# Kernel optimization log

Hardware: AMD Instinct MI355X
Metric: run time of the kernel (lower is better)

Reference implementation:

```python
import jax, jax.numpy as jnp
import numpy as np

T, H = 2048, 1024          # tokens, hidden_size
NH, NKV, D = 16, 4, 64     # heads, kv heads, head_dim
E, F = 8, 1024             # experts, intermediate_size
TOPK = 1
EPS = 1e-5
THETA = 500000.0
SCALE = D ** -0.5


def rmsnorm(x, w=None, eps=EPS):
    # fp32 accumulation like vLLM RMSNorm
    v = jnp.mean(x.astype(jnp.float32) ** 2, axis=-1, keepdims=True)
    y = x.astype(jnp.float32) * jax.lax.rsqrt(v + eps)
    y = y.astype(x.dtype)
    return y * w if w is not None else y


def setup_inputs() -> dict:
    key = jax.random.key(0)
    ks = jax.random.split(key, 12)
    s = 1.0 / np.sqrt(H)
    sf = 1.0 / np.sqrt(F)
    return {
        "positions": jnp.arange(T, dtype=jnp.int32),
        "hidden_states": jax.random.normal(ks[0], (T, H), jnp.float32),
        "ln1_w": jnp.ones((H,), jnp.float32),
        "ln2_w": jnp.ones((H,), jnp.float32),
        "wqkv": jax.random.normal(ks[1], (H, (NH + 2 * NKV) * D), jnp.float32) * s,
        "wo": jax.random.normal(ks[2], (NH * D, H), jnp.float32) * s,
        "router_w": jax.random.normal(ks[3], (H, E), jnp.float32) * s,
        "w_gate": jax.random.normal(ks[4], (E, H, F), jnp.float32) * s,
        "w_up": jax.random.normal(ks[5], (E, H, F), jnp.float32) * s,
        "w_down": jax.random.normal(ks[6], (E, F, H), jnp.float32) * sf,
        "sh_gate": jax.random.normal(ks[7], (H, F), jnp.float32) * s,
        "sh_up": jax.random.normal(ks[8], (H, F), jnp.float32) * s,
        "sh_down": jax.random.normal(ks[9], (F, H), jnp.float32) * sf,
    }


def reference(positions, hidden_states, ln1_w, ln2_w, wqkv, wo, router_w,
              w_gate, w_up, w_down, sh_gate, sh_up, sh_down):
    # --- input_layernorm (residual is None on first call) ---
    residual = hidden_states
    h = rmsnorm(hidden_states, ln1_w)

    # --- attention: qkv proj ---
    qkv = h @ wqkv
    q = qkv[:, : NH * D].reshape(T, NH, D)
    k = qkv[:, NH * D: (NH + NKV) * D].reshape(T, NKV, D)
    v = qkv[:, (NH + NKV) * D:].reshape(T, NKV, D)

    # --- neox-style RoPE ---
    half = D // 2
    inv_freq = 1.0 / (THETA ** (jnp.arange(half, dtype=jnp.float32) / half))
    ang = positions.astype(jnp.float32)[:, None] * inv_freq[None, :]
    cos = jnp.cos(ang)[:, None, :]  # [T,1,half]
    sin = jnp.sin(ang)[:, None, :]

    def rope(x):
        x1, x2 = x[..., :half], x[..., half:]
        return jnp.concatenate([x1 * cos - x2 * sin, x2 * cos + x1 * sin], axis=-1)

    q = rope(q)
    k = rope(k)

    # --- fp32 QK-RMSNorm (no weight), applied after RoPE as in source ---
    q = rmsnorm(q)
    k = rmsnorm(k)

    # --- GQA causal attention ---
    n_rep = NH // NKV
    kr = jnp.repeat(k, n_rep, axis=1)  # [T,NH,D]
    vr = jnp.repeat(v, n_rep, axis=1)
    scores = jnp.einsum('thd,shd->hts', q, kr) * SCALE  # [NH,T,T]
    causal = positions[:, None] >= positions[None, :]
    scores = jnp.where(causal[None], scores, -jnp.inf)
    attn = jax.nn.softmax(scores, axis=-1)
    ao = jnp.einsum('hts,shd->thd', attn, vr).reshape(T, NH * D)
    h = ao @ wo

    # --- post_attention_layernorm with fused residual add ---
    x = h + residual
    residual = x
    h = rmsnorm(x, ln2_w)

    # --- MoE: top-1 sigmoid router, router weight applied on input ---
    logits = h @ router_w                      # [T,E]
    score, idx = jax.lax.top_k(logits, TOPK)   # [T,1]
    gate = jax.nn.sigmoid(score.astype(jnp.float32)).astype(h.dtype)
    x_in = h * gate                            # apply_router_weight_on_input
    onehot = (idx == jnp.arange(E)[None, :]).astype(h.dtype)  # [T,E]
    g = jax.nn.silu(jnp.einsum('th,ehf->tef', x_in, w_gate)) \
        * jnp.einsum('th,ehf->tef', x_in, w_up)               # [T,E,F]
    out_e = jnp.einsum('tef,efh->teh', g, w_down)             # [T,E,H]
    routed = jnp.einsum('teh,te->th', out_e, onehot)

    # --- shared expert (SiLU MLP) ---
    shared = (jax.nn.silu(h @ sh_gate) * (h @ sh_up)) @ sh_down

    out = routed + shared
    return (out, residual)
```

## Files before the change

### kernel.cpp

```cpp
#include <hip/hip_runtime.h>
#include <hip/hip_bf16.h>
#include <cmath>
#include <cstdint>

#define T 2048
#define H 1024
#define NH 16
#define NKV 4
#define DH 64
#define NE 8
#define FF 1024
#define QKVN ((NH + 2 * NKV) * DH)
#define EPS 1e-5f
#define ATTN_SCALE 0.125f
#define LOG2E 1.44269504f
#define MBOUND 12.0f
#define ASPLIT 4

typedef short bf16x8 __attribute__((ext_vector_type(8)));
typedef float floatx4 __attribute__((ext_vector_type(4)));

__device__ __forceinline__ void gload16(const void* g, void* l) {
  __builtin_amdgcn_global_load_lds((const __attribute__((address_space(1))) void*)g,
                                   (__attribute__((address_space(3))) void*)l, 16, 0, 0);
}

__global__ __launch_bounds__(256) void rmsnorm1024(const float* __restrict__ x,
                                                   const float* __restrict__ w,
                                                   __hip_bfloat16* __restrict__ yb) {
  int row = blockIdx.x;
  const float4* x4 = (const float4*)(x + (size_t)row * H);
  float4 v = x4[threadIdx.x];
  float s = v.x * v.x + v.y * v.y + v.z * v.z + v.w * v.w;
  #pragma unroll
  for (int o = 32; o; o >>= 1) s += __shfl_down(s, o, 64);
  __shared__ float red[4];
  if ((threadIdx.x & 63) == 0) red[threadIdx.x >> 6] = s;
  __syncthreads();
  s = red[0] + red[1] + red[2] + red[3];
  float inv = rsqrtf(s * (1.0f / (float)H) + EPS);
  float4 wv = ((const float4*)w)[threadIdx.x];
  __hip_bfloat16* yp = yb + (size_t)row * H + threadIdx.x * 4;
  yp[0] = __float2bfloat16(v.x * inv * wv.x);
  yp[1] = __float2bfloat16(v.y * inv * wv.y);
  yp[2] = __float2bfloat16(v.z * inv * wv.z);
  yp[3] = __float2bfloat16(v.w * inv * wv.w);
}

__global__ __launch_bounds__(256) void fused_add_rms(const float* __restrict__ a,
                                                     const float* __restrict__ b,
                                                     float* __restrict__ resid,
                                                     const float* __restrict__ w,
                                                     float* __restrict__ yf,
                                                     __hip_bfloat16* __restrict__ yb) {
  int row = blockIdx.x;
  float4 av = ((const float4*)(a + (size_t)row * H))[threadIdx.x];
  float4 bv = ((const float4*)(b + (size_t)row * H))[threadIdx.x];
  float4 v = make_float4(av.x + bv.x, av.y + bv.y, av.z + bv.z, av.w + bv.w);
  ((float4*)(resid + (size_t)row * H))[threadIdx.x] = v;
  float s = v.x * v.x + v.y * v.y + v.z * v.z + v.w * v.w;
  #pragma unroll
  for (int o = 32; o; o >>= 1) s += __shfl_down(s, o, 64);
  __shared__ float red[4];
  if ((threadIdx.x & 63) == 0) red[threadIdx.x >> 6] = s;
  __syncthreads();
  s = red[0] + red[1] + red[2] + red[3];
  float inv = rsqrtf(s * (1.0f / (float)H) + EPS);
  float4 wv = ((const float4*)w)[threadIdx.x];
  float o0 = v.x * inv * wv.x, o1 = v.y * inv * wv.y, o2 = v.z * inv * wv.z, o3 = v.w * inv * wv.w;
  ((float4*)(yf + (size_t)row * H))[threadIdx.x] = make_float4(o0, o1, o2, o3);
  __hip_bfloat16* yp = yb + (size_t)row * H + threadIdx.x * 4;
  yp[0] = __float2bfloat16(o0);
  yp[1] = __float2bfloat16(o1);
  yp[2] = __float2bfloat16(o2);
  yp[3] = __float2bfloat16(o3);
}

__global__ __launch_bounds__(256) void tcast9(const float* __restrict__ srcE,
                                              const float* __restrict__ srcS,
                                              __hip_bfloat16* __restrict__ dst, int R, int C,
                                              long long srcStride, long long dstStride,
                                              long long sBatch, long long dBatch) {
  int z = blockIdx.z;
  const float* src = (srcS && z == (int)gridDim.z - 1) ? srcS : srcE + (long long)z * sBatch;
  dst += (long long)z * dBatch;
  int c0 = blockIdx.x * 64, r0 = blockIdx.y * 32;
  __shared__ float tile[32][65];
  int tid = threadIdx.x;
  int lr = tid >> 4;
  int lc = (tid & 15) * 4;
  #pragma unroll
  for (int it = 0; it < 2; it++) {
    float4 v = *(const float4*)(src + (long long)(r0 + lr + it * 16) * srcStride + c0 + lc);
    tile[lr + it * 16][lc + 0] = v.x;
    tile[lr + it * 16][lc + 1] = v.y;
    tile[lr + it * 16][lc + 2] = v.z;
    tile[lr + it * 16][lc + 3] = v.w;
  }
  __syncthreads();
  int oc = tid >> 2;
  int rr = (tid & 3) * 8;
  short ov[8];
  #pragma unroll
  for (int i = 0; i < 8; i++) {
    __hip_bfloat16 b = __float2bfloat16(tile[rr + i][oc]);
    ov[i] = *(short*)&b;
  }
  *(bf16x8*)((short*)dst + (long long)(c0 + oc) * dstStride + r0 + rr) = *(bf16x8*)ov;
}

__global__ __launch_bounds__(256) void gemm_bf16(const __hip_bfloat16* __restrict__ A,
                                                 const __hip_bfloat16* __restrict__ A2,
                                                 const __hip_bfloat16* __restrict__ Bt,
                                                 void* __restrict__ Cout, void* __restrict__ Cout2,
                                                 int M, int N, int K, int out_bf16,
                                                 const int* __restrict__ row_offs,
                                                 long long strideB) {
  int e = blockIdx.z;
  bool sh = (A2 != nullptr && e == (int)gridDim.z - 1);
  int rbeg = 0, rend = M;
  const __hip_bfloat16* Ap = A;
  void* Cp = Cout;
  if (sh) {
    Ap = A2; Cp = Cout2;
  } else if (row_offs) {
    rbeg = row_offs[e]; rend = row_offs[e + 1];
  }
  long long m0 = rbeg + (long long)blockIdx.y * 128;
  if (m0 >= rend) return;
  long long n0 = (long long)blockIdx.x * 64;
  const __hip_bfloat16* Bp = Bt + (long long)e * strideB;

  __shared__ unsigned short As[128 * 64];
  __shared__ unsigned short Bs[64 * 64];

  int tid = threadIdx.x;
  int lane = tid & 63, w = tid >> 6;
  int wr = (w >> 1) * 64, wc = (w & 1) * 32;
  int qd = lane >> 4, ln16 = lane & 15;
  int l7 = ln16 & 7;

  floatx4 acc[4][2];
  floatx4 zero = {0.f, 0.f, 0.f, 0.f};
  #pragma unroll
  for (int i = 0; i < 4; i++)
    #pragma unroll
    for (int j = 0; j < 2; j++) acc[i][j] = zero;

  int rowA[4], kcA[4];
  #pragma unroll
  for (int it = 0; it < 4; it++) {
    int chunk = tid + it * 256;
    rowA[it] = chunk >> 3;
    kcA[it] = ((chunk & 7) ^ (rowA[it] & 7)) * 8;
  }

  for (int k0 = 0; k0 < K; k0 += 64) {
    #pragma unroll
    for (int it = 0; it < 4; it++) {
      long long ra = m0 + rowA[it];
      if (ra >= rend) ra = rend - 1;
      gload16(Ap + ra * K + k0 + kcA[it], As + (tid + it * 256) * 8);
    }
    #pragma unroll
    for (int it = 0; it < 2; it++)
      gload16(Bp + (n0 + rowA[it]) * K + k0 + kcA[it], Bs + (tid + it * 256) * 8);
    __syncthreads();
    #pragma unroll
    for (int s = 0; s < 2; s++) {
      bf16x8 af[4], bfr[2];
      #pragma unroll
      for (int i = 0; i < 4; i++) {
        int row = wr + i * 16 + ln16;
        af[i] = *(const bf16x8*)(As + row * 64 + (((s * 4 + qd) ^ l7) * 8));
      }
      #pragma unroll
      for (int j = 0; j < 2; j++) {
        int row = wc + j * 16 + ln16;
        bfr[j] = *(const bf16x8*)(Bs + row * 64 + (((s * 4 + qd) ^ l7) * 8));
      }
      #pragma unroll
      for (int i = 0; i < 4; i++)
        #pragma unroll
        for (int j = 0; j < 2; j++)
          acc[i][j] = __builtin_amdgcn_mfma_f32_16x16x32_bf16(af[i], bfr[j], acc[i][j], 0, 0, 0);
    }
    __syncthreads();
  }

  #pragma unroll
  for (int i = 0; i < 4; i++) {
    #pragma unroll
    for (int r = 0; r < 4; r++) {
      long long gm = m0 + wr + i * 16 + qd * 4 + r;
      if (gm < rend) {
        #pragma unroll
        for (int j = 0; j < 2; j++) {
          long long gn = n0 + wc + j * 16 + ln16;
          float v = acc[i][j][r];
          if (out_bf16)
            ((__hip_bfloat16*)Cp)[gm * N + gn] = __float2bfloat16(v);
          else
            ((float*)Cp)[gm * N + gn] = v;
        }
      }
    }
  }
}

__global__ __launch_bounds__(256) void rope_pack(const float* __restrict__ qkv,
                                                 const int* __restrict__ positions,
                                                 __hip_bfloat16* __restrict__ Qb,
                                                 __hip_bfloat16* __restrict__ Kb) {
  int b = blockIdx.x * 4 + (threadIdx.x >> 6);
  int t = b / (NH + NKV);
  int hh = b % (NH + NKV);
  const float* ptr = qkv + (long long)t * QKVN + hh * DH;
  int d = threadIdx.x & 63;
  float v = ptr[d];
  int fi = d & 31;
  float inv_freq = exp2f(-(float)fi * (18.93156857f / 32.0f));
  float ang = (float)positions[t] * inv_freq;
  float c = __cosf(ang), s = __sinf(ang);
  float other = __shfl_xor(v, 32, 64);
  float r = (d < 32) ? (v * c - other * s) : (v * c + other * s);
  float sq = r * r;
  #pragma unroll
  for (int off = 32; off; off >>= 1) sq += __shfl_xor(sq, off, 64);
  float o = r * rsqrtf(sq * (1.0f / (float)DH) + EPS);
  if (hh < NH)
    Qb[(size_t)t * (NH * DH) + hh * DH + d] = __float2bfloat16(o * (ATTN_SCALE * LOG2E));
  else
    Kb[(size_t)t * (NKV * DH) + (hh - NH) * DH + d] = __float2bfloat16(o);
}

__global__ __launch_bounds__(256) void attn_mfma(const __hip_bfloat16* __restrict__ Qb,
                                                 const __hip_bfloat16* __restrict__ Kb,
                                                 const __hip_bfloat16* __restrict__ VtG,
                                                 float* __restrict__ Opart,
                                                 float* __restrict__ Lpart) {
  int h = blockIdx.y;
  int kvh = h >> 2;
  int qi = blockIdx.x;
  int sp = blockIdx.z;
  int q0 = qi * 64;
  int nt = qi + 1;
  if (sp >= nt) return;

  __shared__ unsigned short Ks[64 * 64];
  __shared__ unsigned short Vs[64 * 64];
  __shared__ unsigned short Ps[4 * 16 * 64];

  int tid = threadIdx.x;
  int lane = tid & 63, w = tid >> 6;
  int qd = lane >> 4, ln16 = lane & 15;
  int l7 = ln16 & 7;
  unsigned short* Pw = Ps + w * 16 * 64;

  int r0 = tid >> 3;
  int sc = ((tid & 7) ^ (r0 & 7)) * 8;

  int tq = q0 + w * 16 + ln16;
  const unsigned short* qp = (const unsigned short*)Qb + (size_t)tq * (NH * DH) + h * DH;
  bf16x8 aq[2];
  aq[0] = *(const bf16x8*)(qp + qd * 8);
  aq[1] = *(const bf16x8*)(qp + 32 + qd * 8);

  bf16x8 ones;
  #pragma unroll
  for (int i = 0; i < 8; i++) ones[i] = (short)0x3F80;

  floatx4 O_[4], accl;
  floatx4 zero = {0.f, 0.f, 0.f, 0.f};
  #pragma unroll
  for (int j = 0; j < 4; j++) O_[j] = zero;
  accl = zero;
  int tq_base = q0 + w * 16 + qd * 4;
  int wave_min_row = q0 + w * 16;

  for (int kt = sp; kt < nt; kt += ASPLIT) {
    int kb = kt * 64;
    gload16((const unsigned short*)Kb + (size_t)(kb + r0) * (NKV * DH) + kvh * DH + sc, Ks + tid * 8);
    gload16((const unsigned short*)Kb + (size_t)(kb + r0 + 32) * (NKV * DH) + kvh * DH + sc, Ks + tid * 8 + 2048);
    gload16((const unsigned short*)VtG + (size_t)(kvh * DH + r0) * T + kb + sc, Vs + tid * 8);
    gload16((const unsigned short*)VtG + (size_t)(kvh * DH + r0 + 32) * T + kb + sc, Vs + tid * 8 + 2048);
    __syncthreads();

    floatx4 S_[4];
    #pragma unroll
    for (int j = 0; j < 4; j++) S_[j] = zero;
    #pragma unroll
    for (int s = 0; s < 2; s++) {
      bf16x8 bk[4];
      #pragma unroll
      for (int j = 0; j < 4; j++)
        bk[j] = *(const bf16x8*)(Ks + (j * 16 + ln16) * 64 + (((s * 4 + qd) ^ l7) * 8));
      #pragma unroll
      for (int j = 0; j < 4; j++)
        S_[j] = __builtin_amdgcn_mfma_f32_16x16x32_bf16(aq[s], bk[j], S_[j], 0, 0, 0);
    }

    if (kb + 63 > wave_min_row) {
      #pragma unroll
      for (int j = 0; j < 4; j++) {
        int tk = kb + j * 16 + ln16;
        #pragma unroll
        for (int r = 0; r < 4; r++)
          S_[j][r] = (tk <= tq_base + r) ? exp2f(S_[j][r] - MBOUND) : 0.f;
      }
    } else {
      #pragma unroll
      for (int j = 0; j < 4; j++)
        #pragma unroll
        for (int r = 0; r < 4; r++) S_[j][r] = exp2f(S_[j][r] - MBOUND);
    }

    #pragma unroll
    for (int j = 0; j < 4; j++)
      #pragma unroll
      for (int r = 0; r < 4; r++) {
        int row = qd * 4 + r;
        int pc = (((j * 2 + (ln16 >> 3)) ^ (row & 7)) * 8) + l7;
        __hip_bfloat16 pb = __float2bfloat16(S_[j][r]);
        Pw[row * 64 + pc] = *(unsigned short*)&pb;
      }

    #pragma unroll
    for (int s = 0; s < 2; s++) {
      bf16x8 ap = *(const bf16x8*)(Pw + ln16 * 64 + (((s * 4 + qd) ^ l7) * 8));
      bf16x8 bv[4];
      #pragma unroll
      for (int j = 0; j < 4; j++)
        bv[j] = *(const bf16x8*)(Vs + (j * 16 + ln16) * 64 + (((s * 4 + qd) ^ l7) * 8));
      #pragma unroll
      for (int j = 0; j < 4; j++)
        O_[j] = __builtin_amdgcn_mfma_f32_16x16x32_bf16(ap, bv[j], O_[j], 0, 0, 0);
      accl = __builtin_amdgcn_mfma_f32_16x16x32_bf16(ap, ones, accl, 0, 0, 0);
    }
    __syncthreads();
  }

  size_t pbase = ((size_t)(qi * NH + h) * ASPLIT + sp) * (64 * 64);
  int rl_base = w * 16 + qd * 4;
  #pragma unroll
  for (int j = 0; j < 4; j++)
    #pragma unroll
    for (int r = 0; r < 4; r++)
      Opart[pbase + (size_t)(rl_base + r) * 64 + j * 16 + ln16] = O_[j][r];
  if (ln16 == 0) {
    size_t lbase = ((size_t)(qi * NH + h) * ASPLIT + sp) * 64;
    #pragma unroll
    for (int r = 0; r < 4; r++) Lpart[lbase + rl_base + r] = accl[r];
  }
}

__global__ __launch_bounds__(256) void attn_combine(const float* __restrict__ Opart,
                                                    const float* __restrict__ Lpart,
                                                    __hip_bfloat16* __restrict__ ao) {
  int qi = blockIdx.x, h = blockIdx.y;
  int nv = (qi + 1 < ASPLIT) ? (qi + 1) : ASPLIT;
  int row = threadIdx.x >> 2;
  int c0 = (threadIdx.x & 3) * 16;
  size_t base = (size_t)(qi * NH + h) * ASPLIT * 4096;
  size_t lb = (size_t)(qi * NH + h) * ASPLIT * 64;
  float l = 0.f;
  float acc[16];
  #pragma unroll
  for (int i = 0; i < 16; i++) acc[i] = 0.f;
  for (int s = 0; s < nv; s++) {
    const float* Op = Opart + base + (size_t)s * 4096 + (size_t)row * 64 + c0;
    l += Lpart[lb + s * 64 + row];
    #pragma unroll
    for (int i = 0; i < 16; i += 4) {
      float4 v = *(const float4*)(Op + i);
      acc[i] += v.x; acc[i + 1] += v.y; acc[i + 2] += v.z; acc[i + 3] += v.w;
    }
  }
  float inv = 1.f / l;
  int t = qi * 64 + row;
  short ov[16];
  #pragma unroll
  for (int i = 0; i < 16; i++) {
    __hip_bfloat16 b = __float2bfloat16(acc[i] * inv);
    ov[i] = *(short*)&b;
  }
  short* dst = (short*)ao + (size_t)t * (NH * DH) + h * DH + c0;
  *(bf16x8*)dst = *(bf16x8*)&ov[0];
  *(bf16x8*)(dst + 8) = *(bf16x8*)&ov[8];
}

__global__ void silumul_both(const __hip_bfloat16* __restrict__ gA2,
                             const __hip_bfloat16* __restrict__ gS2,
                             __hip_bfloat16* __restrict__ gP,
                             __hip_bfloat16* __restrict__ gPs, int n4each) {
  int i = blockIdx.x * blockDim.x + threadIdx.x;
  const __hip_bfloat16* src = gA2;
  __hip_bfloat16* dst = gP;
  if (i >= n4each) {
    i -= n4each;
    src = gS2;
    dst = gPs;
  }
  int el = i * 4;
  int row = el >> 10;
  int c = el & (FF - 1);
  const __hip_bfloat16* g = src + (size_t)row * (2 * FF) + c;
  #pragma unroll
  for (int k = 0; k < 4; k++) {
    float av = __bfloat162float(g[k]);
    float bv = __bfloat162float(g[FF + k]);
    dst[el + k] = __float2bfloat16(av / (1.f + __expf(-av)) * bv);
  }
}

__global__ __launch_bounds__(64) void router_kernel(const float* __restrict__ h2,
                                                    const float* __restrict__ rw,
                                                    int* __restrict__ idx,
                                                    float* __restrict__ gate,
                                                    int* __restrict__ counts) {
  int t = blockIdx.x;
  int lane = threadIdx.x;
  float acc[NE] = {};
  for (int k = lane; k < H; k += 64) {
    float hv = h2[(long long)t * H + k];
    float4 r0 = *(const float4*)(rw + (long long)k * NE);
    float4 r1 = *(const float4*)(rw + (long long)k * NE + 4);
    acc[0] += hv * r0.x; acc[1] += hv * r0.y; acc[2] += hv * r0.z; acc[3] += hv * r0.w;
    acc[4] += hv * r1.x; acc[5] += hv * r1.y; acc[6] += hv * r1.z; acc[7] += hv * r1.w;
  }
  #pragma unroll
  for (int off = 32; off; off >>= 1)
    #pragma unroll
    for (int e2 = 0; e2 < NE; e2++) acc[e2] += __shfl_down(acc[e2], off, 64);
  if (lane == 0) {
    int best = 0;
    float bv = acc[0];
    #pragma unroll
    for (int e2 = 1; e2 < NE; e2++)
      if (acc[e2] > bv) { bv = acc[e2]; best = e2; }
    idx[t] = best;
    gate[t] = 1.f / (1.f + expf(-bv));
    atomicAdd(&counts[best], 1);
  }
}

__global__ void zero_counts_kernel(int* c) {
  if (threadIdx.x < 2 * NE) c[threadIdx.x] = 0;
}

__global__ void scan_kernel(const int* __restrict__ counts, int* __restrict__ offs) {
  if (threadIdx.x == 0) {
    int s = 0;
    for (int e2 = 0; e2 < NE; e2++) { offs[e2] = s; s += counts[e2]; }
    offs[NE] = s;
  }
}

__global__ void assign_kernel(const int* __restrict__ idx, const int* __restrict__ offs,
                              int* __restrict__ cnt2, int* __restrict__ perm,
                              int* __restrict__ pos) {
  int t = blockIdx.x * blockDim.x + threadIdx.x;
  if (t >= T) return;
  int e2 = idx[t];
  int p = offs[e2] + atomicAdd(&cnt2[e2], 1);
  pos[t] = p;
  perm[p] = t;
}

__global__ __launch_bounds__(256) void gather_kernel(const float* __restrict__ h2,
                                                     const float* __restrict__ gate,
                                                     const int* __restrict__ perm,
                                                     __hip_bfloat16* __restrict__ xg) {
  int p = blockIdx.x;
  int t = perm[p];
  float g = gate[t];
  float4 v = ((const float4*)(h2 + (long long)t * H))[threadIdx.x];
  __hip_bfloat16* yp = xg + (long long)p * H + threadIdx.x * 4;
  yp[0] = __float2bfloat16(v.x * g);
  yp[1] = __float2bfloat16(v.y * g);
  yp[2] = __float2bfloat16(v.z * g);
  yp[3] = __float2bfloat16(v.w * g);
}

__global__ __launch_bounds__(256) void final_add_kernel(float* __restrict__ out,
                                                        const float* __restrict__ outp,
                                                        const int* __restrict__ pos) {
  int t = blockIdx.x;
  int p = pos[t];
  const float4* src = (const float4*)(outp + (long long)p * H);
  float4* dst = (float4*)(out + (long long)t * H);
  float4 a = dst[threadIdx.x];
  float4 b = src[threadIdx.x];
  a.x += b.x; a.y += b.y; a.z += b.z; a.w += b.w;
  dst[threadIdx.x] = a;
}

extern "C" void kernel_launch(void* const* d_in, const int* in_sizes, int n_in,
                              void* d_out, int out_size, void* d_ws, size_t ws_size,
                              hipStream_t stream) {
  const int* positions = (const int*)d_in[0];
  const float* hidden = (const float*)d_in[1];
  const float* ln1_w = (const float*)d_in[2];
  const float* ln2_w = (const float*)d_in[3];
  const float* wqkv = (const float*)d_in[4];
  const float* wo = (const float*)d_in[5];
  const float* router_w = (const float*)d_in[6];
  const float* w_gate = (const float*)d_in[7];
  const float* w_up = (const float*)d_in[8];
  const float* w_down = (const float*)d_in[9];
  const float* sh_gate = (const float*)d_in[10];
  const float* sh_up = (const float*)d_in[11];
  const float* sh_down = (const float*)d_in[12];

  float* out = (float*)d_out;
  float* resid = out + (size_t)T * H;

  char* p = (char*)d_ws;
  auto alloc = [&](size_t bytes) { char* r = p; p += (bytes + 255) & ~(size_t)255; return r; };

  float* qkv = (float*)alloc((size_t)T * QKVN * 4);
  float* h2 = (float*)alloc((size_t)T * H * 4);
  float* gb1 = (float*)alloc((size_t)T * H * 4);
  float* outp = (float*)alloc((size_t)T * H * 4);
  __hip_bfloat16* h1b = (__hip_bfloat16*)alloc((size_t)T * H * 2);
  __hip_bfloat16* aob = (__hip_bfloat16*)alloc((size_t)T * H * 2);
  __hip_bfloat16* h2b = (__hip_bfloat16*)alloc((size_t)T * H * 2);
  __hip_bfloat16* xgb = (__hip_bfloat16*)alloc((size_t)T * H * 2);
  __hip_bfloat16* gA2 = (__hip_bfloat16*)alloc((size_t)T * 2 * FF * 2);
  __hip_bfloat16* gP = (__hip_bfloat16*)alloc((size_t)T * FF * 2);
  __hip_bfloat16* Qb = (__hip_bfloat16*)alloc((size_t)T * NH * DH * 2);
  __hip_bfloat16* Kb = (__hip_bfloat16*)alloc((size_t)T * NKV * DH * 2);
  __hip_bfloat16* VtG = (__hip_bfloat16*)alloc((size_t)NKV * DH * T * 2);
  __hip_bfloat16* wqkvT = (__hip_bfloat16*)alloc((size_t)H * QKVN * 2);
  __hip_bfloat16* woT = (__hip_bfloat16*)alloc((size_t)H * H * 2);
  __hip_bfloat16* wguT = (__hip_bfloat16*)alloc((size_t)9 * 2 * FF * H * 2);
  __hip_bfloat16* wdT = (__hip_bfloat16*)alloc((size_t)9 * H * FF * 2);
  int* counts = (int*)alloc(2 * NE * 4);
  int* cnt2 = counts + NE;
  int* offs = (int*)alloc((NE + 1) * 4);
  int* idx = (int*)alloc(T * 4);
  int* perm = (int*)alloc(T * 4);
  int* pos = (int*)alloc(T * 4);
  float* gate = (float*)alloc(T * 4);

  __hip_bfloat16* gS2 = (__hip_bfloat16*)gb1;
  __hip_bfloat16* gPs = h1b;

  float* Opart = qkv;
  float* Lpart = qkv + (size_t)(T / 64) * NH * ASPLIT * 4096;

  tcast9<<<dim3(QKVN / 64, H / 32, 1), 256, 0, stream>>>(wqkv, nullptr, wqkvT, H, QKVN, QKVN, H, 0, 0);
  tcast9<<<dim3(H / 64, H / 32, 1), 256, 0, stream>>>(wo, nullptr, woT, H, H, H, H, 0, 0);
  tcast9<<<dim3(FF / 64, H / 32, 9), 256, 0, stream>>>(w_gate, sh_gate, wguT, H, FF, FF, H,
                                                       (long long)H * FF, (long long)2 * H * FF);
  tcast9<<<dim3(FF / 64, H / 32, 9), 256, 0, stream>>>(w_up, sh_up, wguT + (size_t)FF * H, H, FF, FF, H,
                                                       (long long)H * FF, (long long)2 * H * FF);
  tcast9<<<dim3(H / 64, FF / 32, 9), 256, 0, stream>>>(w_down, sh_down, wdT, FF, H, H, FF,
                                                       (long long)FF * H, (long long)H * FF);

  rmsnorm1024<<<T, 256, 0, stream>>>(hidden, ln1_w, h1b);
  gemm_bf16<<<dim3(QKVN / 64, T / 128, 1), 256, 0, stream>>>(h1b, nullptr, wqkvT, qkv, nullptr,
                                                             T, QKVN, H, 0, nullptr, 0);
  rope_pack<<<T * (NH + NKV) / 4, 256, 0, stream>>>(qkv, positions, Qb, Kb);
  tcast9<<<dim3(NKV * DH / 64, T / 32, 1), 256, 0, stream>>>(qkv + (NH + NKV) * DH, nullptr, VtG,
                                                             T, NKV * DH, QKVN, T, 0, 0);
  attn_mfma<<<dim3(T / 64, NH, ASPLIT), 256, 0, stream>>>(Qb, Kb, VtG, Opart, Lpart);
  attn_combine<<<dim3(T / 64, NH), 256, 0, stream>>>(Opart, Lpart, aob);
  gemm_bf16<<<dim3(H / 64, T / 128, 1), 256, 0, stream>>>(aob, nullptr, woT, gb1, nullptr,
                                                          T, H, H, 0, nullptr, 0);
  fused_add_rms<<<T, 256, 0, stream>>>(gb1, hidden, resid, ln2_w, h2, h2b);
  zero_counts_kernel<<<1, 64, 0, stream>>>(counts);
  router_kernel<<<T, 64, 0, stream>>>(h2, router_w, idx, gate, counts);
  scan_kernel<<<1, 64, 0, stream>>>(counts, offs);
  assign_kernel<<<T / 256, 256, 0, stream>>>(idx, offs, cnt2, perm, pos);
  gather_kernel<<<T, 256, 0, stream>>>(h2, gate, perm, xgb);
  gemm_bf16<<<dim3(2 * FF / 64, T / 128, 9), 256, 0, stream>>>(xgb, h2b, wguT, gA2, gS2,
                                                               T, 2 * FF, H, 1, offs,
                                                               (long long)2 * H * FF);
  silumul_both<<<(2 * T * FF / 4) / 256, 256, 0, stream>>>(gA2, gS2, gP, gPs, T * FF / 4);
  gemm_bf16<<<dim3(H / 64, T / 128, 9), 256, 0, stream>>>(gP, gPs, wdT, outp, out,
                                                          T, H, FF, 0, offs, (long long)FF * H);
  final_add_kernel<<<T, 256, 0, stream>>>(out, outp, pos);
}
```

Before: 405.6 us.

## Share K/V tiles across GQA heads per block and double-buffer K/V loads

The attention kernel now launches one block per KV head instead of per query head, with each of the four waves handling one query head of the group and all 64 query rows. A K/V tile loaded into LDS is therefore reused by four heads, cutting global K/V traffic by four. K/V loads are also double-buffered so the next tile's copy overlaps compute on the current one. In exchange the grid shrinks by four, each wave does four times the work with much larger register state (64 accumulator floats plus Q fragments), and occupancy may drop despite the launch bound hint.

```diff
diff --git a/kernel.cpp b/kernel.cpp
--- a/kernel.cpp
+++ b/kernel.cpp
@@ -234,25 +234,25 @@
     Kb[(size_t)t * (NKV * DH) + (hh - NH) * DH + d] = __float2bfloat16(o);
 }
 
-__global__ __launch_bounds__(256) void attn_mfma(const __hip_bfloat16* __restrict__ Qb,
-                                                 const __hip_bfloat16* __restrict__ Kb,
-                                                 const __hip_bfloat16* __restrict__ VtG,
-                                                 float* __restrict__ Opart,
-                                                 float* __restrict__ Lpart) {
-  int h = blockIdx.y;
-  int kvh = h >> 2;
+__global__ __launch_bounds__(256, 2) void attn_mfma(const __hip_bfloat16* __restrict__ Qb,
+                                                    const __hip_bfloat16* __restrict__ Kb,
+                                                    const __hip_bfloat16* __restrict__ VtG,
+                                                    float* __restrict__ Opart,
+                                                    float* __restrict__ Lpart) {
+  int kvh = blockIdx.y;
   int qi = blockIdx.x;
   int sp = blockIdx.z;
   int q0 = qi * 64;
   int nt = qi + 1;
   if (sp >= nt) return;
 
-  __shared__ unsigned short Ks[64 * 64];
-  __shared__ unsigned short Vs[64 * 64];
+  __shared__ unsigned short Ks[2][64 * 64];
+  __shared__ unsigned short Vs[2][64 * 64];
   __shared__ unsigned short Ps[4 * 16 * 64];
 
   int tid = threadIdx.x;
   int lane = tid & 63, w = tid >> 6;
+  int h = kvh * 4 + w;
   int qd = lane >> 4, ln16 = lane & 15;
   int l7 = ln16 & 7;
   unsigned short* Pw = Ps + w * 16 * 64;
@@ -260,97 +260,128 @@
   int r0 = tid >> 3;
   int sc = ((tid & 7) ^ (r0 & 7)) * 8;
 
-  int tq = q0 + w * 16 + ln16;
-  const unsigned short* qp = (const unsigned short*)Qb + (size_t)tq * (NH * DH) + h * DH;
-  bf16x8 aq[2];
-  aq[0] = *(const bf16x8*)(qp + qd * 8);
-  aq[1] = *(const bf16x8*)(qp + 32 + qd * 8);
+  bf16x8 aq[4][2];
+  #pragma unroll
+  for (int rt = 0; rt < 4; rt++) {
+    const unsigned short* qp =
+        (const unsigned short*)Qb + (size_t)(q0 + rt * 16 + ln16) * (NH * DH) + h * DH;
+    aq[rt][0] = *(const bf16x8*)(qp + qd * 8);
+    aq[rt][1] = *(const bf16x8*)(qp + 32 + qd * 8);
+  }
 
   bf16x8 ones;
   #pragma unroll
   for (int i = 0; i < 8; i++) ones[i] = (short)0x3F80;
 
-  floatx4 O_[4], accl;
+  floatx4 O_[4][4], accl[4];
   floatx4 zero = {0.f, 0.f, 0.f, 0.f};
   #pragma unroll
-  for (int j = 0; j < 4; j++) O_[j] = zero;
-  accl = zero;
-  int tq_base = q0 + w * 16 + qd * 4;
-  int wave_min_row = q0 + w * 16;
-
+  for (int rt = 0; rt < 4; rt++) {
+    #pragma unroll
+    for (int j = 0; j < 4; j++) O_[rt][j] = zero;
+    accl[rt] = zero;
+  }
+
+  {
+    int kb = sp * 64;
+    gload16((const unsigned short*)Kb + (size_t)(kb + r0) * (NKV * DH) + kvh * DH + sc, Ks[0] + tid * 8);
+    gload16((const unsigned short*)Kb + (size_t)(kb + r0 + 32) * (NKV * DH) + kvh * DH + sc, Ks[0] + tid * 8 + 2048);
+    gload16((const unsigned short*)VtG + (size_t)(kvh * DH + r0) * T + kb + sc, Vs[0] + tid * 8);
+    gload16((const unsigned short*)VtG + (size_t)(kvh * DH + r0 + 32) * T + kb + sc, Vs[0] + tid * 8 + 2048);
+  }
+  __syncthreads();
+
+  int cur = 0;
   for (int kt = sp; kt < nt; kt += ASPLIT) {
+    int ktn = kt + ASPLIT;
+    if (ktn < nt) {
+      int kb = ktn * 64;
+      unsigned short* Kn = Ks[cur ^ 1];
+      unsigned short* Vn = Vs[cur ^ 1];
+      gload16((const unsigned short*)Kb + (size_t)(kb + r0) * (NKV * DH) + kvh * DH + sc, Kn + tid * 8);
+      gload16((const unsigned short*)Kb + (size_t)(kb + r0 + 32) * (NKV * DH) + kvh * DH + sc, Kn + tid * 8 + 2048);
+      gload16((const unsigned short*)VtG + (size_t)(kvh * DH + r0) * T + kb + sc, Vn + tid * 8);
+      gload16((const unsigned short*)VtG + (size_t)(kvh * DH + r0 + 32) * T + kb + sc, Vn + tid * 8 + 2048);
+    }
+    const unsigned short* Kc = Ks[cur];
+    const unsigned short* Vc = Vs[cur];
     int kb = kt * 64;
-    gload16((const unsigned short*)Kb + (size_t)(kb + r0) * (NKV * DH) + kvh * DH + sc, Ks + tid * 8);
-    gload16((const unsigned short*)Kb + (size_t)(kb + r0 + 32) * (NKV * DH) + kvh * DH + sc, Ks + tid * 8 + 2048);
-    gload16((const unsigned short*)VtG + (size_t)(kvh * DH + r0) * T + kb + sc, Vs + tid * 8);
-    gload16((const unsigned short*)VtG + (size_t)(kvh * DH + r0 + 32) * T + kb + sc, Vs + tid * 8 + 2048);
-    __syncthreads();
-
-    floatx4 S_[4];
-    #pragma unroll
-    for (int j = 0; j < 4; j++) S_[j] = zero;
-    #pragma unroll
-    for (int s = 0; s < 2; s++) {
-      bf16x8 bk[4];
+
+    #pragma unroll
+    for (int rt = 0; rt < 4; rt++) {
+      floatx4 S_[4];
+      #pragma unroll
+      for (int j = 0; j < 4; j++) S_[j] = zero;
+      #pragma unroll
+      for (int s = 0; s < 2; s++) {
+        bf16x8 bk[4];
+        #pragma unroll
+        for (int j = 0; j < 4; j++)
+          bk[j] = *(const bf16x8*)(Kc + (j * 16 + ln16) * 64 + (((s * 4 + qd) ^ l7) * 8));
+        #pragma unroll
+        for (int j = 0; j < 4; j++)
+          S_[j] = __builtin_amdgcn_mfma_f32_16x16x32_bf16(aq[rt][s], bk[j], S_[j], 0, 0, 0);
+      }
+
+      int tq_base = q0 + rt * 16 + qd * 4;
+      if (kb + 63 > q0 + rt * 16) {
+        #pragma unroll
+        for (int j = 0; j < 4; j++) {
+          int tk = kb + j * 16 + ln16;
+          #pragma unroll
+          for (int r = 0; r < 4; r++)
+            S_[j][r] = (tk <= tq_base + r) ? exp2f(S_[j][r] - MBOUND) : 0.f;
+        }
+      } else {
+        #pragma unroll
+        for (int j = 0; j < 4; j++)
+          #pragma unroll
+          for (int r = 0; r < 4; r++) S_[j][r] = exp2f(S_[j][r] - MBOUND);
+      }
+
       #pragma unroll
       for (int j = 0; j < 4; j++)
-        bk[j] = *(const bf16x8*)(Ks + (j * 16 + ln16) * 64 + (((s * 4 + qd) ^ l7) * 8));
-      #pragma unroll
-      for (int j = 0; j < 4; j++)
-        S_[j] = __builtin_amdgcn_mfma_f32_16x16x32_bf16(aq[s], bk[j], S_[j], 0, 0, 0);
-    }
-
-    if (kb + 63 > wave_min_row) {
-      #pragma unroll
-      for (int j = 0; j < 4; j++) {
-        int tk = kb + j * 16 + ln16;
-        #pragma unroll
-        for (int r = 0; r < 4; r++)
-          S_[j][r] = (tk <= tq_base + r) ? exp2f(S_[j][r] - MBOUND) : 0.f;
+        #pragma unroll
+        for (int r = 0; r < 4; r++) {
+          int row = qd * 4 + r;
+          int pc = (((j * 2 + (ln16 >> 3)) ^ (row & 7)) * 8) + l7;
+          __hip_bfloat16 pb = __float2bfloat16(S_[j][r]);
+          Pw[row * 64 + pc] = *(unsigned short*)&pb;
+        }
+
+      #pragma unroll
+      for (int s = 0; s < 2; s++) {
+        bf16x8 ap = *(const bf16x8*)(Pw + ln16 * 64 + (((s * 4 + qd) ^ l7) * 8));
+        bf16x8 bv[4];
+        #pragma unroll
+        for (int j = 0; j < 4; j++)
+          bv[j] = *(const bf16x8*)(Vc + (j * 16 + ln16) * 64 + (((s * 4 + qd) ^ l7) * 8));
+        #pragma unroll
+        for (int j = 0; j < 4; j++)
+          O_[rt][j] = __builtin_amdgcn_mfma_f32_16x16x32_bf16(ap, bv[j], O_[rt][j], 0, 0, 0);
+        accl[rt] = __builtin_amdgcn_mfma_f32_16x16x32_bf16(ap, ones, accl[rt], 0, 0, 0);
       }
-    } else {
-      #pragma unroll
-      for (int j = 0; j < 4; j++)
-        #pragma unroll
-        for (int r = 0; r < 4; r++) S_[j][r] = exp2f(S_[j][r] - MBOUND);
-    }
-
-    #pragma unroll
-    for (int j = 0; j < 4; j++)
-      #pragma unroll
-      for (int r = 0; r < 4; r++) {
-        int row = qd * 4 + r;
-        int pc = (((j * 2 + (ln16 >> 3)) ^ (row & 7)) * 8) + l7;
-        __hip_bfloat16 pb = __float2bfloat16(S_[j][r]);
-        Pw[row * 64 + pc] = *(unsigned short*)&pb;
-      }
-
-    #pragma unroll
-    for (int s = 0; s < 2; s++) {
-      bf16x8 ap = *(const bf16x8*)(Pw + ln16 * 64 + (((s * 4 + qd) ^ l7) * 8));
-      bf16x8 bv[4];
-      #pragma unroll
-      for (int j = 0; j < 4; j++)
-        bv[j] = *(const bf16x8*)(Vs + (j * 16 + ln16) * 64 + (((s * 4 + qd) ^ l7) * 8));
-      #pragma unroll
-      for (int j = 0; j < 4; j++)
-        O_[j] = __builtin_amdgcn_mfma_f32_16x16x32_bf16(ap, bv[j], O_[j], 0, 0, 0);
-      accl = __builtin_amdgcn_mfma_f32_16x16x32_bf16(ap, ones, accl, 0, 0, 0);
     }
     __syncthreads();
+    cur ^= 1;
   }
 
   size_t pbase = ((size_t)(qi * NH + h) * ASPLIT + sp) * (64 * 64);
-  int rl_base = w * 16 + qd * 4;
-  #pragma unroll
-  for (int j = 0; j < 4; j++)
-    #pragma unroll
-    for (int r = 0; r < 4; r++)
-      Opart[pbase + (size_t)(rl_base + r) * 64 + j * 16 + ln16] = O_[j][r];
+  #pragma unroll
+  for (int rt = 0; rt < 4; rt++) {
+    int rl_base = rt * 16 + qd * 4;
+    #pragma unroll
+    for (int j = 0; j < 4; j++)
+      #pragma unroll
+      for (int r = 0; r < 4; r++)
+        Opart[pbase + (size_t)(rl_base + r) * 64 + j * 16 + ln16] = O_[rt][j][r];
+  }
   if (ln16 == 0) {
     size_t lbase = ((size_t)(qi * NH + h) * ASPLIT + sp) * 64;
     #pragma unroll
-    for (int r = 0; r < 4; r++) Lpart[lbase + rl_base + r] = accl[r];
+    for (int rt = 0; rt < 4; rt++)
+      #pragma unroll
+      for (int r = 0; r < 4; r++) Lpart[lbase + rt * 16 + qd * 4 + r] = accl[rt][r];
   }
 }
 
@@ -564,7 +595,7 @@
   rope_pack<<<T * (NH + NKV) / 4, 256, 0, stream>>>(qkv, positions, Qb, Kb);
   tcast9<<<dim3(NKV * DH / 64, T / 32, 1), 256, 0, stream>>>(qkv + (NH + NKV) * DH, nullptr, VtG,
                                                              T, NKV * DH, QKVN, T, 0, 0);
-  attn_mfma<<<dim3(T / 64, NH, ASPLIT), 256, 0, stream>>>(Qb, Kb, VtG, Opart, Lpart);
+  attn_mfma<<<dim3(T / 64, NKV, ASPLIT), 256, 0, stream>>>(Qb, Kb, VtG, Opart, Lpart);
   attn_combine<<<dim3(T / 64, NH), 256, 0, stream>>>(Opart, Lpart, aob);
   gemm_bf16<<<dim3(H / 64, T / 128, 1), 256, 0, stream>>>(aob, nullptr, woT, gb1, nullptr,
                                                           T, H, H, 0, nullptr, 0);
```

After: 409.3 us. Within noise of the previous version (+0.9%).
